# Kernel optimization log

Measured on AMD Instinct MI355X. Metric: run time of the kernel, lower is better.

The kernel has to match this reference:

```python
import jax, jax.numpy as jnp
import numpy as np


def setup_inputs() -> dict:
    key = jax.random.key(0)
    ks = jax.random.split(key, 7)
    B, N, Fin, Fout = 32, 1024, 64, 64
    s = 1.0 / np.sqrt(Fin)
    return {
        "X": jax.random.normal(ks[0], (B, N, Fin), dtype=jnp.float32),
        "A": jax.random.normal(ks[1], (B, N, N), dtype=jnp.float32),  # unused in forward, kept for signature fidelity
        "W": jax.random.uniform(ks[2], (Fin, Fout), jnp.float32, -s, s),
        "att_W": jax.random.uniform(ks[3], (Fin, Fout), jnp.float32, -s, s),
        "a": jax.random.uniform(ks[4], (Fout, Fout), jnp.float32, -s, s),
        "bias_W": jax.random.uniform(ks[5], (Fout,), jnp.float32, -s, s),
        "self_W": jax.random.uniform(ks[6], (Fin, Fout), jnp.float32, -s, s),
    }


def reference(X, A, W, att_W, a, bias_W, self_W):
    # att_X = X @ att_W : [B, N, Fout]
    att_X = jnp.einsum('bnf,fg->bng', X, att_W)
    # torch einsum 'ij,ajk->ajk' sums `a` over i => per-feature scale a.sum(0)
    scale = jnp.sum(a, axis=0)  # [Fout]
    # Z[b,i,k] = sum_j att_X[b,i,j] * scale[j] * att_X[b,k,j]  -> [B, N, N]
    Z = jnp.einsum('big,bkg->bik', att_X * scale, att_X)
    n = Z.shape[1]
    Z = Z * (1.0 - jnp.eye(n, dtype=Z.dtype))  # zero diagonal per batch
    att = jax.nn.leaky_relu(Z, negative_slope=0.01)
    # H = att @ (X W) + bias_W + X self_W
    XW = jnp.einsum('bnf,fg->bng', X, W)
    H = jnp.einsum('bnm,bmg->bng', att, XW) + bias_W
    H = H + jnp.einsum('bnf,fg->bng', X, self_W)
    return H
```

## Files before the change

kernel.cpp:

```cpp
#include <hip/hip_runtime.h>

#define DEV __device__ __forceinline__
typedef short s16x8 __attribute__((ext_vector_type(8)));
typedef float f32x16 __attribute__((ext_vector_type(16)));
typedef unsigned short u16;

#define WAIT_VMCNT(N) asm volatile("s_waitcnt vmcnt(" #N ")" ::: "memory")
#define CFENCE asm volatile("" ::: "memory")

DEV unsigned cvt_pk_bf16(float lo, float hi) {
  unsigned r;
  asm volatile("v_cvt_pk_bf16_f32 %0, %1, %2" : "=v"(r) : "v"(lo), "v"(hi));
  return r;
}
DEV u16 f2bf(float f) {
  unsigned u = __builtin_bit_cast(unsigned, f);
  unsigned r = u + 0x7fffu + ((u >> 16) & 1u);
  return (u16)(r >> 16);
}
DEV float bf2f(u16 u) { return __builtin_bit_cast(float, (unsigned)u << 16); }
DEV f32x16 zero16() {
  f32x16 v;
  #pragma unroll
  for (int i = 0; i < 16; ++i) v[i] = 0.f;
  return v;
}

DEV void gld16(const u16* g, u16* l) {
  __builtin_amdgcn_global_load_lds(
      (const __attribute__((address_space(1))) void*)g,
      (__attribute__((address_space(3))) void*)l, 16, 0, 0);
}

DEV void stage_tile64(const u16* __restrict__ gbase, size_t stride, u16* lbuf, int t) {
  #pragma unroll
  for (int p = 0; p < 2; ++p) {
    int c = p * 256 + t;
    int row = c >> 3, s = c & 7;
    int gck = s ^ (row & 7);
    const u16* src = gbase + (size_t)row * stride + gck * 8;
    u16* dst = lbuf + (size_t)(p * 256 + (t & 192)) * 8;
    gld16(src, dst);
  }
}

DEV s16x8 frag(const u16* buf, int row, int chunk) {
  return *(const s16x8*)(buf + row * 64 + ((chunk ^ (row & 7)) << 3));
}

DEV int kswz(int row, int d) {
  return row * 64 + ((((d >> 3) ^ (row & 7)) << 3) | (d & 7));
}

DEV void stage_wt(const float* __restrict__ src, u16* dst, int t) {
  #pragma unroll
  for (int r = 0; r < 4; ++r) {
    int e = (r * 256 + t) * 4;
    int f = e >> 6, g0 = e & 63;
    float4 v = *(const float4*)(src + f * 64 + g0);
    float vv[4] = {v.x, v.y, v.z, v.w};
    #pragma unroll
    for (int j = 0; j < 4; ++j) {
      int g = g0 + j;
      dst[g * 64 + ((((f >> 3) ^ (g & 7)) << 3) | (f & 7))] = f2bf(vv[j]);
    }
  }
}

__global__ __launch_bounds__(256) void prep_kernel(
    const float* __restrict__ X, const float* __restrict__ W,
    const float* __restrict__ attW, const float* __restrict__ Aa,
    const float* __restrict__ biasW, const float* __restrict__ selfW,
    u16* __restrict__ Kbf, u16* __restrict__ Vt, u16* __restrict__ Bb,
    float* __restrict__ scal_ws) {
  __shared__ __align__(16) u16 Xl[64 * 64];
  __shared__ __align__(16) u16 Wt[3][64 * 64];
  __shared__ __align__(16) u16 Bl[64 * 64];
  __shared__ __align__(16) u16 Vl[64 * 72];
  __shared__ float sc4[4][64];

  const int t = threadIdx.x;
  const int b = blockIdx.x;
  const int n0 = blockIdx.y * 64;
  const int r0 = b * 1024 + n0;
  const bool sblk = (blockIdx.x == 0 && blockIdx.y == 0);
  const int lane = t & 63, w = t >> 6, h = lane >> 5, ln = lane & 31;
  const int rg = (w >> 1) * 32;
  const int cf = w & 1;
  const int d = cf * 32 + ln;

  if (sblk) {
    int qt = t >> 6, dd = t & 63;
    float s = 0.f;
    #pragma unroll
    for (int i = 0; i < 16; ++i) s += Aa[(qt * 16 + i) * 64 + dd];
    sc4[qt][dd] = s;
  }

  #pragma unroll
  for (int p = 0; p < 2; ++p) {
    int c = p * 256 + t;
    int row = c >> 3, ck = c & 7;
    const float4* src = (const float4*)(X + (size_t)(r0 + row) * 64 + ck * 8);
    float4 a0 = src[0], a1 = src[1];
    unsigned* dst = (unsigned*)&Xl[row * 64 + ((ck ^ (row & 7)) << 3)];
    dst[0] = cvt_pk_bf16(a0.x, a0.y);
    dst[1] = cvt_pk_bf16(a0.z, a0.w);
    dst[2] = cvt_pk_bf16(a1.x, a1.y);
    dst[3] = cvt_pk_bf16(a1.z, a1.w);
  }
  stage_wt(attW, &Wt[0][0], t);
  stage_wt(W, &Wt[1][0], t);
  stage_wt(selfW, &Wt[2][0], t);
  __syncthreads();

  s16x8 xa[4];
  #pragma unroll
  for (int ks = 0; ks < 4; ++ks) xa[ks] = frag(Xl, rg + ln, ks * 2 + h);

  f32x16 aA = zero16(), aW = zero16(), aS = zero16();
  #pragma unroll
  for (int ks = 0; ks < 4; ++ks) {
    s16x8 bA = frag(&Wt[0][0], d, ks * 2 + h);
    s16x8 bW = frag(&Wt[1][0], d, ks * 2 + h);
    s16x8 bS = frag(&Wt[2][0], d, ks * 2 + h);
    aA = __builtin_amdgcn_mfma_f32_32x32x16_bf16(xa[ks], bA, aA, 0, 0, 0);
    aW = __builtin_amdgcn_mfma_f32_32x32x16_bf16(xa[ks], bW, aW, 0, 0, 0);
    aS = __builtin_amdgcn_mfma_f32_32x32x16_bf16(xa[ks], bS, aS, 0, 0, 0);
  }
  __syncthreads();

  const float bi = biasW[d];
  #pragma unroll
  for (int reg = 0; reg < 16; ++reg) {
    int rl = (reg & 3) + 8 * (reg >> 2) + 4 * h;
    int row = rg + rl;
    Xl[kswz(row, d)] = f2bf(aA[reg]);
    Bl[kswz(row, d)] = f2bf(aS[reg] + bi);
  }
  #pragma unroll
  for (int pg = 0; pg < 4; ++pg) {
    int n = rg + pg * 8 + 4 * h;
    *(unsigned*)&Vl[d * 72 + n] = cvt_pk_bf16(aW[pg * 4 + 0], aW[pg * 4 + 1]);
    *(unsigned*)&Vl[d * 72 + n + 2] = cvt_pk_bf16(aW[pg * 4 + 2], aW[pg * 4 + 3]);
  }
  __syncthreads();

  #pragma unroll
  for (int p = 0; p < 2; ++p) {
    int c = p * 256 + t;
    int row = c >> 3, ck = c & 7;
    size_t go = (size_t)(r0 + row) * 64 + ck * 8;
    int lo = row * 64 + ((ck ^ (row & 7)) << 3);
    *(s16x8*)&Kbf[go] = *(const s16x8*)&Xl[lo];
    *(s16x8*)&Bb[go] = *(const s16x8*)&Bl[lo];
  }
  #pragma unroll
  for (int p = 0; p < 2; ++p) {
    int c = p * 256 + t;
    int dd = c >> 3, ck = c & 7;
    *(s16x8*)&Vt[(size_t)(b * 64 + dd) * 1024 + n0 + ck * 8] =
        *(const s16x8*)&Vl[dd * 72 + ck * 8];
  }
  if (sblk && t < 64)
    scal_ws[t] = sc4[0][t] + sc4[1][t] + sc4[2][t] + sc4[3][t];
}

#define PROC(SV, DG, PWV)                                                      \
  do {                                                                         \
    float p_[16];                                                              \
    _Pragma("unroll") for (int r_ = 0; r_ < 16; ++r_) {                        \
      float v_ = (SV)[r_];                                                     \
      p_[r_] = fmaxf(v_, 0.f) + 0.01f * fminf(v_, 0.f);                        \
    }                                                                          \
    if (DG) {                                                                  \
      _Pragma("unroll") for (int r_ = 0; r_ < 16; ++r_) {                      \
        int rl_ = (r_ & 3) + 8 * (r_ >> 2) + 4 * h;                            \
        p_[r_] = (rl_ == ln) ? 0.f : p_[r_];                                   \
      }                                                                        \
    }                                                                          \
    unsigned pk_[8];                                                           \
    _Pragma("unroll") for (int i_ = 0; i_ < 8; ++i_)                           \
        pk_[i_] = cvt_pk_bf16(p_[2 * i_], p_[2 * i_ + 1]);                     \
    auto a0_ = __builtin_amdgcn_permlane32_swap(pk_[0], pk_[2], false, false); \
    auto a1_ = __builtin_amdgcn_permlane32_swap(pk_[1], pk_[3], false, false); \
    auto a2_ = __builtin_amdgcn_permlane32_swap(pk_[4], pk_[6], false, false); \
    auto a3_ = __builtin_amdgcn_permlane32_swap(pk_[5], pk_[7], false, false); \
    PWV[0][0] = a0_[0]; PWV[0][1] = a1_[0]; PWV[0][2] = a0_[1];                \
    PWV[0][3] = a1_[1]; PWV[1][0] = a2_[0]; PWV[1][1] = a3_[0];                \
    PWV[1][2] = a2_[1]; PWV[1][3] = a3_[1];                                    \
  } while (0)

__global__ __launch_bounds__(256) void attn_kernel(
    const u16* __restrict__ Kbf, const u16* __restrict__ Vt,
    const u16* __restrict__ Bb, const float* __restrict__ scal_ws,
    float* __restrict__ Hout) {
  __shared__ __align__(16) u16 ring[3][2][4096];

  const int t = threadIdx.x;
  const int b = blockIdx.x;
  const int q0 = blockIdx.y * 128;
  const int lane = t & 63, w = t >> 6, h = lane >> 5, ln = lane & 31;
  const int qb = q0 + w * 32;

  const u16* Kg = Kbf + (size_t)b * 65536;
  const u16* Vg = Vt + (size_t)b * 65536;

  stage_tile64(Kg, 64, &ring[0][0][0], t);
  stage_tile64(Vg, 1024, &ring[0][1][0], t);
  stage_tile64(Kg + (size_t)64 * 64, 64, &ring[1][0][0], t);
  stage_tile64(Vg + 64, 1024, &ring[1][1][0], t);

  s16x8 qf[4];
  #pragma unroll
  for (int ks = 0; ks < 4; ++ks) {
    s16x8 raw = *(const s16x8*)(Kg + (size_t)(qb + ln) * 64 + ks * 16 + h * 8);
    float4 sA = *(const float4*)(scal_ws + ks * 16 + h * 8);
    float4 sB = *(const float4*)(scal_ws + ks * 16 + h * 8 + 4);
    union { unsigned u[4]; s16x8 v; } qq;
    qq.u[0] = cvt_pk_bf16(bf2f((u16)raw[0]) * sA.x, bf2f((u16)raw[1]) * sA.y);
    qq.u[1] = cvt_pk_bf16(bf2f((u16)raw[2]) * sA.z, bf2f((u16)raw[3]) * sA.w);
    qq.u[2] = cvt_pk_bf16(bf2f((u16)raw[4]) * sB.x, bf2f((u16)raw[5]) * sB.y);
    qq.u[3] = cvt_pk_bf16(bf2f((u16)raw[6]) * sB.z, bf2f((u16)raw[7]) * sB.w);
    qf[ks] = qq.v;
  }

  f32x16 o0 = zero16(), o1 = zero16();

  #pragma unroll 1
  for (int tix = 0; tix < 16; ++tix) {
    const int kv0 = tix * 64;
    if (tix < 15) {
      WAIT_VMCNT(4);
    } else {
      WAIT_VMCNT(0);
    }
    __builtin_amdgcn_s_barrier();
    CFENCE;
    if (tix < 14) {
      const int ns = (tix + 2) % 3;
      stage_tile64(Kg + (size_t)(kv0 + 128) * 64, 64, &ring[ns][0][0], t);
      stage_tile64(Vg + (kv0 + 128), 1024, &ring[ns][1][0], t);
    }
    const u16* Kl = &ring[tix % 3][0][0];
    const u16* Vl = &ring[tix % 3][1][0];

    f32x16 s0 = zero16(), s1 = zero16();
    __builtin_amdgcn_s_setprio(1);
    #pragma unroll
    for (int ks = 0; ks < 4; ++ks) {
      s0 = __builtin_amdgcn_mfma_f32_32x32x16_bf16(frag(Kl, ln, ks * 2 + h), qf[ks], s0, 0, 0, 0);
      s1 = __builtin_amdgcn_mfma_f32_32x32x16_bf16(frag(Kl, 32 + ln, ks * 2 + h), qf[ks], s1, 0, 0, 0);
    }
    __builtin_amdgcn_s_setprio(0);

    const bool dg0 = (kv0 == qb);
    const bool dg1 = (kv0 + 32 == qb);
    unsigned pw0[2][4], pw1[2][4];
    PROC(s0, dg0, pw0);
    PROC(s1, dg1, pw1);

    __builtin_amdgcn_s_setprio(1);
    #pragma unroll
    for (int c = 0; c < 4; ++c) {
      union { unsigned u[4]; s16x8 v; } pb;
      pb.u[0] = (c < 2 ? pw0 : pw1)[c & 1][0];
      pb.u[1] = (c < 2 ? pw0 : pw1)[c & 1][1];
      pb.u[2] = (c < 2 ? pw0 : pw1)[c & 1][2];
      pb.u[3] = (c < 2 ? pw0 : pw1)[c & 1][3];
      o0 = __builtin_amdgcn_mfma_f32_32x32x16_bf16(frag(Vl, ln, c * 2 + h), pb.v, o0, 0, 0, 0);
      o1 = __builtin_amdgcn_mfma_f32_32x32x16_bf16(frag(Vl, 32 + ln, c * 2 + h), pb.v, o1, 0, 0, 0);
    }
    __builtin_amdgcn_s_setprio(0);
  }

  __syncthreads();

  float* Ow = (float*)&ring[0][0][0] + (size_t)w * 2048;
  #pragma unroll
  for (int reg = 0; reg < 16; ++reg) {
    int rl = (reg & 3) + 8 * (reg >> 2) + 4 * h;
    int d0 = rl, d1 = 32 + rl;
    Ow[ln * 64 + ((((d0 >> 2) ^ (ln & 15)) << 2) | (d0 & 3))] = o0[reg];
    Ow[ln * 64 + ((((d1 >> 2) ^ (ln & 15)) << 2) | (d1 & 3))] = o1[reg];
  }
  #pragma unroll
  for (int p = 0; p < 8; ++p) {
    int row = p * 4 + (lane >> 4);
    int g = lane & 15;
    int off = row * 64 + ((g ^ (row & 15)) << 2);
    float4 v = *(const float4*)&Ow[off];
    size_t go = ((size_t)b * 1024 + qb + row) * 64 + g * 4;
    const short4 bv = *(const short4*)(Bb + go);
    v.x += bf2f((u16)bv.x);
    v.y += bf2f((u16)bv.y);
    v.z += bf2f((u16)bv.z);
    v.w += bf2f((u16)bv.w);
    *(float4*)(Hout + go) = v;
  }
}

extern "C" void kernel_launch(void* const* d_in, const int* in_sizes, int n_in,
                              void* d_out, int out_size, void* d_ws, size_t ws_size,
                              hipStream_t stream) {
  const float* X = (const float*)d_in[0];
  const float* W = (const float*)d_in[2];
  const float* attW = (const float*)d_in[3];
  const float* a = (const float*)d_in[4];
  const float* biasW = (const float*)d_in[5];
  const float* selfW = (const float*)d_in[6];
  float* H = (float*)d_out;

  u16* Kbf = (u16*)d_ws;
  u16* Vt = Kbf + (size_t)32 * 1024 * 64;
  u16* Bb = Vt + (size_t)32 * 1024 * 64;
  float* scal = (float*)(Bb + (size_t)32 * 1024 * 64);

  prep_kernel<<<dim3(32, 16), 256, 0, stream>>>(X, W, attW, a, biasW, selfW,
                                                Kbf, Vt, Bb, scal);
  attn_kernel<<<dim3(32, 8), 256, 0, stream>>>(Kbf, Vt, Bb, scal, H);
}
```

Baseline: 34.39 us.

## Deepen KV ring to four stages and stagger tile start per block

The LDS ring buffer grows from three to four slots, with three tiles prefetched ahead instead of two, and the vmcnt waits are adjusted to match. Each block also starts its KV sweep at a different tile offset derived from the query tile and batch index. This is meant to hide more global-load latency and spread concurrent blocks across different K/V tiles. The cost is more shared memory per block, which may lower occupancy.

```diff
diff --git a/kernel.cpp b/kernel.cpp
--- a/kernel.cpp
+++ b/kernel.cpp
@@ -195,21 +195,25 @@
     const u16* __restrict__ Kbf, const u16* __restrict__ Vt,
     const u16* __restrict__ Bb, const float* __restrict__ scal_ws,
     float* __restrict__ Hout) {
-  __shared__ __align__(16) u16 ring[3][2][4096];
+  __shared__ __align__(16) u16 ring[4][2][4096];
 
   const int t = threadIdx.x;
   const int b = blockIdx.x;
-  const int q0 = blockIdx.y * 128;
+  const int qt = blockIdx.y;
+  const int q0 = qt * 128;
   const int lane = t & 63, w = t >> 6, h = lane >> 5, ln = lane & 31;
   const int qb = q0 + w * 32;
+  const int start = ((qt << 1) + (b >> 3)) & 15;
 
   const u16* Kg = Kbf + (size_t)b * 65536;
   const u16* Vg = Vt + (size_t)b * 65536;
 
-  stage_tile64(Kg, 64, &ring[0][0][0], t);
-  stage_tile64(Vg, 1024, &ring[0][1][0], t);
-  stage_tile64(Kg + (size_t)64 * 64, 64, &ring[1][0][0], t);
-  stage_tile64(Vg + 64, 1024, &ring[1][1][0], t);
+  #pragma unroll
+  for (int i = 0; i < 3; ++i) {
+    int tt = (start + i) & 15;
+    stage_tile64(Kg + (size_t)tt * 64 * 64, 64, &ring[i][0][0], t);
+    stage_tile64(Vg + tt * 64, 1024, &ring[i][1][0], t);
+  }
 
   s16x8 qf[4];
   #pragma unroll
@@ -228,22 +232,26 @@
   f32x16 o0 = zero16(), o1 = zero16();
 
   #pragma unroll 1
-  for (int tix = 0; tix < 16; ++tix) {
-    const int kv0 = tix * 64;
-    if (tix < 15) {
+  for (int i = 0; i < 16; ++i) {
+    const int tt = (start + i) & 15;
+    const int kv0 = tt * 64;
+    if (i <= 13) {
+      WAIT_VMCNT(8);
+    } else if (i == 14) {
       WAIT_VMCNT(4);
     } else {
       WAIT_VMCNT(0);
     }
     __builtin_amdgcn_s_barrier();
     CFENCE;
-    if (tix < 14) {
-      const int ns = (tix + 2) % 3;
-      stage_tile64(Kg + (size_t)(kv0 + 128) * 64, 64, &ring[ns][0][0], t);
-      stage_tile64(Vg + (kv0 + 128), 1024, &ring[ns][1][0], t);
-    }
-    const u16* Kl = &ring[tix % 3][0][0];
-    const u16* Vl = &ring[tix % 3][1][0];
+    if (i < 13) {
+      const int nt_ = (start + i + 3) & 15;
+      const int ns = (i + 3) & 3;
+      stage_tile64(Kg + (size_t)nt_ * 64 * 64, 64, &ring[ns][0][0], t);
+      stage_tile64(Vg + nt_ * 64, 1024, &ring[ns][1][0], t);
+    }
+    const u16* Kl = &ring[i & 3][0][0];
+    const u16* Vl = &ring[i & 3][1][0];
 
     f32x16 s0 = zero16(), s1 = zero16();
     __builtin_amdgcn_s_setprio(1);
```

New measurement: 34.33 us. Within noise of the previous version (-0.2%).
